# Optimization experiments

Measured on AMD Instinct MI355X. Metric: run time of the kernel, lower is better.

The kernel has to match this reference:

```python
import jax, jax.numpy as jnp
import numpy as np

B, S, D, H, DFF = 4, 2048, 1024, 16, 4096
HD = D // H
EPS = 1e-12

def _layernorm(x, g, b):
    mu = jnp.mean(x, axis=-1, keepdims=True)
    var = jnp.mean(jnp.square(x - mu), axis=-1, keepdims=True)
    return (x - mu) * jax.lax.rsqrt(var + EPS) * g + b

def setup_inputs() -> dict:
    key = jax.random.key(0)
    ks = jax.random.split(key, 12)
    sd = 0.02
    inp = {
        'hidden_states': jax.random.normal(ks[0], (B, S, D), jnp.float32),
        'attention_mask': jnp.zeros((B, 1, 1, S), jnp.float32),
        'Wq': jax.random.normal(ks[1], (D, D), jnp.float32) * sd,
        'bq': jnp.zeros((D,), jnp.float32),
        'Wk': jax.random.normal(ks[2], (D, D), jnp.float32) * sd,
        'bk': jnp.zeros((D,), jnp.float32),
        'Wv': jax.random.normal(ks[3], (D, D), jnp.float32) * sd,
        'bv': jnp.zeros((D,), jnp.float32),
        'Wo': jax.random.normal(ks[4], (D, D), jnp.float32) * sd,
        'bo': jnp.zeros((D,), jnp.float32),
        'ln1_g': jnp.ones((D,), jnp.float32),
        'ln1_b': jnp.zeros((D,), jnp.float32),
        'Wi': jax.random.normal(ks[5], (D, DFF), jnp.float32) * sd,
        'bi': jnp.zeros((DFF,), jnp.float32),
        'Wo2': jax.random.normal(ks[6], (DFF, D), jnp.float32) * sd,
        'bo2': jnp.zeros((D,), jnp.float32),
        'ln2_g': jnp.ones((D,), jnp.float32),
        'ln2_b': jnp.zeros((D,), jnp.float32),
    }
    return inp

def reference(hidden_states, attention_mask, Wq, bq, Wk, bk, Wv, bv, Wo, bo,
              ln1_g, ln1_b, Wi, bi, Wo2, bo2, ln2_g, ln2_b):
    x = hidden_states  # [B,S,D]
    # project and split heads -> [B,H,S,hd]
    def heads(t):
        return t.reshape(B, S, H, HD).transpose(0, 2, 1, 3)
    q = heads(x @ Wq + bq)
    k = heads(x @ Wk + bk)
    v = heads(x @ Wv + bv)
    scores = jnp.einsum('bhqd,bhkd->bhqk', q, k) / np.float32(np.sqrt(HD))
    scores = scores + attention_mask  # additive mask broadcast [B,1,1,S]
    weights = jax.nn.softmax(scores, axis=-1)
    ctx = jnp.einsum('bhqk,bhkd->bhqd', weights, v)
    ctx = ctx.transpose(0, 2, 1, 3).reshape(B, S, D)
    attn_out = _layernorm(ctx @ Wo + bo + x, ln1_g, ln1_b)
    # FFN (gelu) with residual + LayerNorm
    h = jax.nn.gelu(attn_out @ Wi + bi, approximate=False)
    out = _layernorm(h @ Wo2 + bo2 + attn_out, ln2_g, ln2_b)
    return out
```

## Files before the change

### kernel.cpp

```cpp
#include <hip/hip_runtime.h>
#include <hip/hip_bf16.h>
#include <math.h>

#define B_   4
#define S_   2048
#define D_   1024
#define H_   16
#define HD_  64
#define DFF_ 4096
#define M_   (B_*S_)

typedef __bf16 bf16x8 __attribute__((ext_vector_type(8)));
typedef __bf16 bf16x4 __attribute__((ext_vector_type(4)));
typedef float  floatx4 __attribute__((ext_vector_type(4)));

__device__ __forceinline__ float  b2f(__bf16 v) { return (float)v; }
__device__ __forceinline__ __bf16 f2b(float v)  { return (__bf16)v; }

__device__ __forceinline__ void async_ld16(const void* g, void* l) {
    __builtin_amdgcn_global_load_lds(
        (const __attribute__((address_space(1))) unsigned int*)g,
        (__attribute__((address_space(3))) unsigned int*)l, 16, 0, 0);
}

__global__ void transpose_conv_kernel(const float* __restrict__ in,
                                      __bf16* __restrict__ out, int R, int C,
                                      float scale)
{
    __shared__ float t[32][33];
    int c0 = blockIdx.x * 32, r0 = blockIdx.y * 32;
    int tx = threadIdx.x, ty = threadIdx.y;
    for (int i = ty; i < 32; i += 8)
        t[i][tx] = in[(long)(r0 + i) * C + c0 + tx];
    __syncthreads();
    for (int i = ty; i < 32; i += 8)
        out[(long)(c0 + i) * R + r0 + tx] = f2b(t[tx][i] * scale);
}

__global__ void vt_transpose_kernel(const __bf16* __restrict__ qkv,
                                    __bf16* __restrict__ vtg)
{
    __shared__ __bf16 t[32][34];
    int b  = blockIdx.z;
    int h  = blockIdx.y >> 1;
    int d0 = (blockIdx.y & 1) * 32;
    int s0 = blockIdx.x * 32;
    int tx = threadIdx.x, ty = threadIdx.y;
    for (int i = ty; i < 32; i += 8)
        t[i][tx] = qkv[(long)(b * S_ + s0 + i) * 3072 + 2048 + h * 64 + d0 + tx];
    __syncthreads();
    for (int i = ty; i < 32; i += 8)
        vtg[((long)(b * H_ + h) * 64 + d0 + i) * S_ + s0 + tx] = t[tx][i];
}

__global__ void f2b_kernel(const float* __restrict__ in, __bf16* __restrict__ out,
                           long n)
{
    long i = ((long)blockIdx.x * 256 + threadIdx.x) * 8;
    if (i >= n) return;
    float4 a = *(const float4*)&in[i];
    float4 c = *(const float4*)&in[i + 4];
    union { __bf16 h[8]; uint4 u; } p;
    p.h[0] = f2b(a.x); p.h[1] = f2b(a.y); p.h[2] = f2b(a.z); p.h[3] = f2b(a.w);
    p.h[4] = f2b(c.x); p.h[5] = f2b(c.y); p.h[6] = f2b(c.z); p.h[7] = f2b(c.w);
    *(uint4*)&out[i] = p.u;
}

__global__ void bias_concat_kernel(const float* __restrict__ bq,
                                   const float* __restrict__ bk,
                                   const float* __restrict__ bv,
                                   float* __restrict__ dst)
{
    int i = blockIdx.x * 256 + threadIdx.x;
    if (i >= 3 * D_) return;
    float v = (i < D_) ? bq[i] * 0.125f
            : (i < 2 * D_) ? bk[i - D_] : bv[i - 2 * D_];
    dst[i] = v;
}

template<int MODE>
__global__ __launch_bounds__(256, 2)
void gemm_kernel(const __bf16* __restrict__ A, const __bf16* __restrict__ Bt,
                 const float* __restrict__ bias, const float* __restrict__ resid,
                 float* __restrict__ Cf, __bf16* __restrict__ Cb,
                 int M, int N, int K)
{
    __shared__ __bf16 sA[128 * 64];
    __shared__ __bf16 sB[128 * 64];

    const int tid  = threadIdx.x;
    const int lane = tid & 63;
    const int wave = tid >> 6;
    const int wm   = (wave >> 1) * 64;
    const int wn   = (wave & 1) * 64;
    const long bm  = (long)blockIdx.y * 128;
    const long bn  = (long)blockIdx.x * 128;

    floatx4 acc[4][4];
#pragma unroll
    for (int i = 0; i < 4; ++i)
#pragma unroll
        for (int j = 0; j < 4; ++j)
#pragma unroll
            for (int r = 0; r < 4; ++r) acc[i][j][r] = 0.0f;

    const int mrow = lane & 15;
    const int quad = lane >> 4;
    const int koff0 = ((0 * 4 + quad) ^ (mrow & 7)) * 8;
    const int koff1 = ((1 * 4 + quad) ^ (mrow & 7)) * 8;

    for (int k0 = 0; k0 < K; k0 += 64) {
        __syncthreads();
#pragma unroll
        for (int t = 0; t < 4; ++t) {
            int ci  = tid + t * 256;
            int row = ci >> 3;
            int col = ((ci & 7) ^ (row & 7)) << 3;
            async_ld16(A  + (bm + row) * (long)K + k0 + col, &sA[ci * 8]);
            async_ld16(Bt + (bn + row) * (long)K + k0 + col, &sB[ci * 8]);
        }
        __syncthreads();

#pragma unroll
        for (int s = 0; s < 2; ++s) {
            const int ko = s ? koff1 : koff0;
            bf16x8 a[4], b[4];
#pragma unroll
            for (int i = 0; i < 4; ++i)
                a[i] = *(const bf16x8*)&sA[(wm + i * 16 + mrow) * 64 + ko];
#pragma unroll
            for (int j = 0; j < 4; ++j)
                b[j] = *(const bf16x8*)&sB[(wn + j * 16 + mrow) * 64 + ko];
#pragma unroll
            for (int i = 0; i < 4; ++i)
#pragma unroll
                for (int j = 0; j < 4; ++j)
                    acc[i][j] = __builtin_amdgcn_mfma_f32_16x16x32_bf16(
                        a[i], b[j], acc[i][j], 0, 0, 0);
        }
    }

    const int rq = quad * 4;
    const int cn = lane & 15;
#pragma unroll
    for (int i = 0; i < 4; ++i) {
#pragma unroll
        for (int j = 0; j < 4; ++j) {
            long col = bn + wn + j * 16 + cn;
            float bv = bias[col];
#pragma unroll
            for (int r = 0; r < 4; ++r) {
                long row = bm + wm + i * 16 + rq + r;
                float v = acc[i][j][r] + bv;
                if (MODE == 0) {
                    Cb[row * N + col] = f2b(v);
                } else if (MODE == 1) {
                    Cf[row * N + col] = v + resid[row * N + col];
                } else {
                    float g = 0.5f * v * (1.0f + erff(v * 0.70710678118654752f));
                    Cb[row * N + col] = f2b(g);
                }
            }
        }
    }
}

__global__ __launch_bounds__(256, 2)
void attn_kernel(const __bf16* __restrict__ QKV, const __bf16* __restrict__ VT,
                 const float* __restrict__ mask, __bf16* __restrict__ ctx)
{
    __shared__ __bf16 Qs[64 * 64];
    __shared__ __bf16 Ks[64 * 64];
    __shared__ __bf16 Vt[64 * 64];
    __shared__ __bf16 Ps[64 * 64];

    const int tid  = threadIdx.x;
    const int lane = tid & 63;
    const int wave = tid >> 6;
    const int w16  = wave * 16;
    const int b    = blockIdx.z, h = blockIdx.y;
    const int q0   = blockIdx.x * 64;
    const int cn   = lane & 15;
    const int quad = lane >> 4;
    const int rq   = quad * 4;
    const int koff0 = ((0 * 4 + quad) ^ (cn & 7)) * 8;
    const int koff1 = ((1 * 4 + quad) ^ (cn & 7)) * 8;

#pragma unroll
    for (int t = 0; t < 2; ++t) {
        int ci = tid + t * 256;
        int qr = ci >> 3, dc = ((ci & 7) ^ (qr & 7)) << 3;
        async_ld16(QKV + (long)(b * S_ + q0 + qr) * 3072 + h * 64 + dc,
                   &Qs[ci * 8]);
    }
    __syncthreads();
    const bf16x8 aq0 = *(const bf16x8*)&Qs[(w16 + cn) * 64 + koff0];
    const bf16x8 aq1 = *(const bf16x8*)&Qs[(w16 + cn) * 64 + koff1];

    float l_[4];
    floatx4 o_[4];
#pragma unroll
    for (int r = 0; r < 4; ++r) l_[r] = 0.0f;
#pragma unroll
    for (int jt = 0; jt < 4; ++jt)
#pragma unroll
        for (int r = 0; r < 4; ++r) o_[jt][r] = 0.0f;

    const long vbase = ((long)(b * H_ + h) * 64) * S_;

    for (int k0 = 0; k0 < S_; k0 += 64) {
        __syncthreads();
#pragma unroll
        for (int t = 0; t < 2; ++t) {
            int ci = tid + t * 256;
            int kr = ci >> 3, dc = ((ci & 7) ^ (kr & 7)) << 3;
            async_ld16(QKV + (long)(b * S_ + k0 + kr) * 3072 + 1024 + h * 64 + dc,
                       &Ks[ci * 8]);
            int vd = ci >> 3, kc = ((ci & 7) ^ (vd & 7)) << 3;
            async_ld16(VT + vbase + (long)vd * S_ + k0 + kc, &Vt[ci * 8]);
        }
        __syncthreads();

        floatx4 st[4];
#pragma unroll
        for (int jt = 0; jt < 4; ++jt)
#pragma unroll
            for (int r = 0; r < 4; ++r) st[jt][r] = 0.0f;
#pragma unroll
        for (int jt = 0; jt < 4; ++jt) {
            bf16x8 b0 = *(const bf16x8*)&Ks[(jt * 16 + cn) * 64 + koff0];
            bf16x8 b1 = *(const bf16x8*)&Ks[(jt * 16 + cn) * 64 + koff1];
            st[jt] = __builtin_amdgcn_mfma_f32_16x16x32_bf16(aq0, b0, st[jt], 0, 0, 0);
            st[jt] = __builtin_amdgcn_mfma_f32_16x16x32_bf16(aq1, b1, st[jt], 0, 0, 0);
        }
#pragma unroll
        for (int jt = 0; jt < 4; ++jt) {
            float mv = mask[(long)b * S_ + k0 + jt * 16 + cn] - 8.0f;
#pragma unroll
            for (int r = 0; r < 4; ++r) {
                float p = __expf(st[jt][r] + mv);
                st[jt][r] = p;
                l_[r] += p;
            }
        }
#pragma unroll
        for (int jt = 0; jt < 4; ++jt)
#pragma unroll
            for (int r = 0; r < 4; ++r) {
                int prow = w16 + rq + r;
                int pcol = (((jt * 2 + (cn >> 3)) ^ (prow & 7)) << 3) + (cn & 7);
                Ps[prow * 64 + pcol] = f2b(st[jt][r]);
            }

        {
            bf16x8 ap0 = *(const bf16x8*)&Ps[(w16 + cn) * 64 + koff0];
            bf16x8 ap1 = *(const bf16x8*)&Ps[(w16 + cn) * 64 + koff1];
#pragma unroll
            for (int jt = 0; jt < 4; ++jt) {
                bf16x8 b0 = *(const bf16x8*)&Vt[(jt * 16 + cn) * 64 + koff0];
                bf16x8 b1 = *(const bf16x8*)&Vt[(jt * 16 + cn) * 64 + koff1];
                o_[jt] = __builtin_amdgcn_mfma_f32_16x16x32_bf16(ap0, b0, o_[jt], 0, 0, 0);
                o_[jt] = __builtin_amdgcn_mfma_f32_16x16x32_bf16(ap1, b1, o_[jt], 0, 0, 0);
            }
        }
    }

#pragma unroll
    for (int r = 0; r < 4; ++r) {
        float l = l_[r];
        l += __shfl_xor(l, 1);
        l += __shfl_xor(l, 2);
        l += __shfl_xor(l, 4);
        l += __shfl_xor(l, 8);
        float linv = 1.0f / l;
        long rowg = (long)(b * S_ + q0 + w16 + rq + r) * D_ + h * 64;
#pragma unroll
        for (int jt = 0; jt < 4; ++jt)
            ctx[rowg + jt * 16 + cn] = f2b(o_[jt][r] * linv);
    }
}

__global__ __launch_bounds__(256)
void ln_kernel(const float* __restrict__ X, const float* __restrict__ gamma,
               const float* __restrict__ beta, float* __restrict__ out,
               __bf16* __restrict__ outb)
{
    const long row = blockIdx.x;
    const int tid = threadIdx.x;
    const float* x = X + row * D_;
    float4 v = *(const float4*)&x[tid * 4];
    float s  = v.x + v.y + v.z + v.w;
    float s2 = v.x * v.x + v.y * v.y + v.z * v.z + v.w * v.w;
    for (int off = 32; off > 0; off >>= 1) {
        s  += __shfl_down(s, off);
        s2 += __shfl_down(s2, off);
    }
    __shared__ float red[8];
    int wave = tid >> 6, lane = tid & 63;
    if (lane == 0) { red[wave] = s; red[4 + wave] = s2; }
    __syncthreads();
    float ts  = red[0] + red[1] + red[2] + red[3];
    float ts2 = red[4] + red[5] + red[6] + red[7];
    float mu  = ts * (1.0f / D_);
    float var = ts2 * (1.0f / D_) - mu * mu;
    float rs  = rsqrtf(fmaxf(var, 0.0f) + 1e-12f);
    float4 g = *(const float4*)&gamma[tid * 4];
    float4 b = *(const float4*)&beta[tid * 4];
    float4 o;
    o.x = (v.x - mu) * rs * g.x + b.x;
    o.y = (v.y - mu) * rs * g.y + b.y;
    o.z = (v.z - mu) * rs * g.z + b.z;
    o.w = (v.w - mu) * rs * g.w + b.w;
    *(float4*)&out[row * D_ + tid * 4] = o;
    if (outb) {
        bf16x4 ob;
        ob[0] = f2b(o.x); ob[1] = f2b(o.y); ob[2] = f2b(o.z); ob[3] = f2b(o.w);
        *(bf16x4*)&outb[row * D_ + tid * 4] = ob;
    }
}

extern "C" void kernel_launch(void* const* d_in, const int* in_sizes, int n_in,
                              void* d_out, int out_size, void* d_ws, size_t ws_size,
                              hipStream_t stream)
{
    const float* hid  = (const float*)d_in[0];
    const float* mask = (const float*)d_in[1];
    const float* Wq   = (const float*)d_in[2];
    const float* bq   = (const float*)d_in[3];
    const float* Wk   = (const float*)d_in[4];
    const float* bk   = (const float*)d_in[5];
    const float* Wv   = (const float*)d_in[6];
    const float* bv   = (const float*)d_in[7];
    const float* Wo   = (const float*)d_in[8];
    const float* bo   = (const float*)d_in[9];
    const float* g1   = (const float*)d_in[10];
    const float* b1   = (const float*)d_in[11];
    const float* Wi   = (const float*)d_in[12];
    const float* bi   = (const float*)d_in[13];
    const float* Wo2  = (const float*)d_in[14];
    const float* bo2  = (const float*)d_in[15];
    const float* g2   = (const float*)d_in[16];
    const float* b2   = (const float*)d_in[17];
    float* out = (float*)d_out;

    char* w = (char*)d_ws;
    auto take = [&](size_t bytes) { char* p = w; w += bytes; return p; };
    __bf16* wqkvb = (__bf16*)take((size_t)3 * D_ * D_ * 2);
    __bf16* wob   = (__bf16*)take((size_t)D_ * D_ * 2);
    __bf16* wib   = (__bf16*)take((size_t)D_ * DFF_ * 2);
    __bf16* wo2b  = (__bf16*)take((size_t)D_ * DFF_ * 2);
    float*  qkvbias = (float*)take(16384);
    __bf16* qkv   = (__bf16*)take((size_t)M_ * 3 * D_ * 2);
    __bf16* ctxb  = (__bf16*)take((size_t)M_ * D_ * 2);
    __bf16* hb    = (__bf16*)take((size_t)M_ * D_ * 2);
    float*  tmp      = (float*)take((size_t)M_ * D_ * 4);
    float*  attn_out = (float*)take((size_t)M_ * D_ * 4);
    __bf16* hbuf = qkv;
    __bf16* vtg  = hb;
    __bf16* attn_out_b = hb;
    (void)in_sizes; (void)n_in; (void)out_size; (void)ws_size;

    dim3 tb(32, 8);
    transpose_conv_kernel<<<dim3(D_/32, D_/32), tb, 0, stream>>>(Wq, wqkvb,            D_, D_, 0.125f);
    transpose_conv_kernel<<<dim3(D_/32, D_/32), tb, 0, stream>>>(Wk, wqkvb + D_*D_,    D_, D_, 1.0f);
    transpose_conv_kernel<<<dim3(D_/32, D_/32), tb, 0, stream>>>(Wv, wqkvb + 2*D_*D_,  D_, D_, 1.0f);
    transpose_conv_kernel<<<dim3(D_/32, D_/32), tb, 0, stream>>>(Wo, wob, D_, D_, 1.0f);
    transpose_conv_kernel<<<dim3(DFF_/32, D_/32), tb, 0, stream>>>(Wi, wib, D_, DFF_, 1.0f);
    transpose_conv_kernel<<<dim3(D_/32, DFF_/32), tb, 0, stream>>>(Wo2, wo2b, DFF_, D_, 1.0f);
    bias_concat_kernel<<<12, 256, 0, stream>>>(bq, bk, bv, qkvbias);
    f2b_kernel<<<(M_*D_/8 + 255)/256, 256, 0, stream>>>(hid, hb, (long)M_*D_);

    gemm_kernel<0><<<dim3(3*D_/128, M_/128), 256, 0, stream>>>(
        hb, wqkvb, qkvbias, nullptr, nullptr, qkv, M_, 3*D_, D_);

    vt_transpose_kernel<<<dim3(S_/32, H_*2, B_), tb, 0, stream>>>(qkv, vtg);

    attn_kernel<<<dim3(S_/64, H_, B_), 256, 0, stream>>>(qkv, vtg, mask, ctxb);

    gemm_kernel<1><<<dim3(D_/128, M_/128), 256, 0, stream>>>(
        ctxb, wob, bo, hid, tmp, nullptr, M_, D_, D_);
    ln_kernel<<<M_, 256, 0, stream>>>(tmp, g1, b1, attn_out, attn_out_b);

    gemm_kernel<2><<<dim3(DFF_/128, M_/128), 256, 0, stream>>>(
        attn_out_b, wib, bi, nullptr, nullptr, hbuf, M_, DFF_, D_);
    gemm_kernel<1><<<dim3(D_/128, M_/128), 256, 0, stream>>>(
        hbuf, wo2b, bo2, attn_out, tmp, nullptr, M_, D_, DFF_);
    ln_kernel<<<M_, 256, 0, stream>>>(tmp, g2, b2, out, nullptr);
}
```

Before: 611.4 us.

## Double-buffer K/V tiles and process 128 queries per attention block

The attention kernel now handles 128 query rows per block (32 per wave, two 16-row MFMA tiles), so each K/V tile loaded into shared memory is reused across twice as many queries. K/V staging is double-buffered: the next tile's async loads are issued before computing on the current one, with one barrier per iteration instead of two. Q is read straight from global memory into registers instead of going through shared memory. In exchange, register pressure and shared memory per block go up, and the grid is half as large (512 blocks), which may reduce occupancy.

```diff
diff --git a/kernel.cpp b/kernel.cpp
--- a/kernel.cpp
+++ b/kernel.cpp
@@ -169,115 +169,152 @@
 void attn_kernel(const __bf16* __restrict__ QKV, const __bf16* __restrict__ VT,
                  const float* __restrict__ mask, __bf16* __restrict__ ctx)
 {
-    __shared__ __bf16 Qs[64 * 64];
-    __shared__ __bf16 Ks[64 * 64];
-    __shared__ __bf16 Vt[64 * 64];
-    __shared__ __bf16 Ps[64 * 64];
+    __shared__ __bf16 Ks[2][64 * 64];
+    __shared__ __bf16 Vt[2][64 * 64];
+    __shared__ __bf16 Ps[128 * 64];
 
     const int tid  = threadIdx.x;
     const int lane = tid & 63;
     const int wave = tid >> 6;
-    const int w16  = wave * 16;
+    const int wq   = wave * 32;
     const int b    = blockIdx.z, h = blockIdx.y;
-    const int q0   = blockIdx.x * 64;
+    const int q0   = blockIdx.x * 128;
     const int cn   = lane & 15;
     const int quad = lane >> 4;
     const int rq   = quad * 4;
     const int koff0 = ((0 * 4 + quad) ^ (cn & 7)) * 8;
     const int koff1 = ((1 * 4 + quad) ^ (cn & 7)) * 8;
 
-#pragma unroll
-    for (int t = 0; t < 2; ++t) {
-        int ci = tid + t * 256;
-        int qr = ci >> 3, dc = ((ci & 7) ^ (qr & 7)) << 3;
-        async_ld16(QKV + (long)(b * S_ + q0 + qr) * 3072 + h * 64 + dc,
-                   &Qs[ci * 8]);
-    }
-    __syncthreads();
-    const bf16x8 aq0 = *(const bf16x8*)&Qs[(w16 + cn) * 64 + koff0];
-    const bf16x8 aq1 = *(const bf16x8*)&Qs[(w16 + cn) * 64 + koff1];
-
-    float l_[4];
-    floatx4 o_[4];
-#pragma unroll
-    for (int r = 0; r < 4; ++r) l_[r] = 0.0f;
-#pragma unroll
-    for (int jt = 0; jt < 4; ++jt)
-#pragma unroll
-        for (int r = 0; r < 4; ++r) o_[jt][r] = 0.0f;
+    bf16x8 aq0[2], aq1[2];
+#pragma unroll
+    for (int it = 0; it < 2; ++it) {
+        const __bf16* qp =
+            QKV + (long)(b * S_ + q0 + wq + it * 16 + cn) * 3072 + h * 64;
+        aq0[it] = *(const bf16x8*)(qp + quad * 8);
+        aq1[it] = *(const bf16x8*)(qp + 32 + quad * 8);
+    }
+
+    float l_[2][4];
+    floatx4 o_[2][4];
+#pragma unroll
+    for (int it = 0; it < 2; ++it) {
+#pragma unroll
+        for (int r = 0; r < 4; ++r) l_[it][r] = 0.0f;
+#pragma unroll
+        for (int jt = 0; jt < 4; ++jt)
+#pragma unroll
+            for (int r = 0; r < 4; ++r) o_[it][jt][r] = 0.0f;
+    }
 
     const long vbase = ((long)(b * H_ + h) * 64) * S_;
 
-    for (int k0 = 0; k0 < S_; k0 += 64) {
-        __syncthreads();
+    auto STAGE = [&](int bufi, int k0) {
 #pragma unroll
         for (int t = 0; t < 2; ++t) {
             int ci = tid + t * 256;
-            int kr = ci >> 3, dc = ((ci & 7) ^ (kr & 7)) << 3;
-            async_ld16(QKV + (long)(b * S_ + k0 + kr) * 3072 + 1024 + h * 64 + dc,
-                       &Ks[ci * 8]);
-            int vd = ci >> 3, kc = ((ci & 7) ^ (vd & 7)) << 3;
-            async_ld16(VT + vbase + (long)vd * S_ + k0 + kc, &Vt[ci * 8]);
-        }
-        __syncthreads();
-
-        floatx4 st[4];
-#pragma unroll
-        for (int jt = 0; jt < 4; ++jt)
-#pragma unroll
-            for (int r = 0; r < 4; ++r) st[jt][r] = 0.0f;
+            int r  = ci >> 3;
+            int cz = ((ci & 7) ^ (r & 7)) << 3;
+            async_ld16(QKV + (long)(b * S_ + k0 + r) * 3072 + 1024 + h * 64 + cz,
+                       &Ks[bufi][ci * 8]);
+            async_ld16(VT + vbase + (long)r * S_ + k0 + cz, &Vt[bufi][ci * 8]);
+        }
+    };
+
+    STAGE(0, 0);
+    asm volatile("s_waitcnt vmcnt(0)" ::: "memory");
+    __builtin_amdgcn_s_barrier();
+    __builtin_amdgcn_sched_barrier(0);
+
+    int cur = 0;
+    for (int k0 = 0; k0 < S_; k0 += 64) {
+        if (k0 + 64 < S_) STAGE(cur ^ 1, k0 + 64);
+
+        floatx4 st[2][4];
+#pragma unroll
+        for (int it = 0; it < 2; ++it)
+#pragma unroll
+            for (int jt = 0; jt < 4; ++jt)
+#pragma unroll
+                for (int r = 0; r < 4; ++r) st[it][jt][r] = 0.0f;
 #pragma unroll
         for (int jt = 0; jt < 4; ++jt) {
-            bf16x8 b0 = *(const bf16x8*)&Ks[(jt * 16 + cn) * 64 + koff0];
-            bf16x8 b1 = *(const bf16x8*)&Ks[(jt * 16 + cn) * 64 + koff1];
-            st[jt] = __builtin_amdgcn_mfma_f32_16x16x32_bf16(aq0, b0, st[jt], 0, 0, 0);
-            st[jt] = __builtin_amdgcn_mfma_f32_16x16x32_bf16(aq1, b1, st[jt], 0, 0, 0);
-        }
+            bf16x8 kb0 = *(const bf16x8*)&Ks[cur][(jt * 16 + cn) * 64 + koff0];
+            bf16x8 kb1 = *(const bf16x8*)&Ks[cur][(jt * 16 + cn) * 64 + koff1];
+#pragma unroll
+            for (int it = 0; it < 2; ++it) {
+                st[it][jt] = __builtin_amdgcn_mfma_f32_16x16x32_bf16(
+                    aq0[it], kb0, st[it][jt], 0, 0, 0);
+                st[it][jt] = __builtin_amdgcn_mfma_f32_16x16x32_bf16(
+                    aq1[it], kb1, st[it][jt], 0, 0, 0);
+            }
+        }
+
 #pragma unroll
         for (int jt = 0; jt < 4; ++jt) {
             float mv = mask[(long)b * S_ + k0 + jt * 16 + cn] - 8.0f;
 #pragma unroll
-            for (int r = 0; r < 4; ++r) {
-                float p = __expf(st[jt][r] + mv);
-                st[jt][r] = p;
-                l_[r] += p;
+            for (int it = 0; it < 2; ++it)
+#pragma unroll
+                for (int r = 0; r < 4; ++r) {
+                    float p = __expf(st[it][jt][r] + mv);
+                    st[it][jt][r] = p;
+                    l_[it][r] += p;
+                }
+        }
+
+#pragma unroll
+        for (int it = 0; it < 2; ++it)
+#pragma unroll
+            for (int jt = 0; jt < 4; ++jt)
+#pragma unroll
+                for (int r = 0; r < 4; ++r) {
+                    int prow = wq + it * 16 + rq + r;
+                    int pcol = (((jt * 2 + (cn >> 3)) ^ (prow & 7)) << 3) + (cn & 7);
+                    Ps[prow * 64 + pcol] = f2b(st[it][jt][r]);
+                }
+
+        {
+            bf16x8 ap0[2], ap1[2];
+#pragma unroll
+            for (int it = 0; it < 2; ++it) {
+                ap0[it] = *(const bf16x8*)&Ps[(wq + it * 16 + cn) * 64 + koff0];
+                ap1[it] = *(const bf16x8*)&Ps[(wq + it * 16 + cn) * 64 + koff1];
             }
-        }
-#pragma unroll
-        for (int jt = 0; jt < 4; ++jt)
-#pragma unroll
-            for (int r = 0; r < 4; ++r) {
-                int prow = w16 + rq + r;
-                int pcol = (((jt * 2 + (cn >> 3)) ^ (prow & 7)) << 3) + (cn & 7);
-                Ps[prow * 64 + pcol] = f2b(st[jt][r]);
+#pragma unroll
+            for (int jt = 0; jt < 4; ++jt) {
+                bf16x8 vb0 = *(const bf16x8*)&Vt[cur][(jt * 16 + cn) * 64 + koff0];
+                bf16x8 vb1 = *(const bf16x8*)&Vt[cur][(jt * 16 + cn) * 64 + koff1];
+#pragma unroll
+                for (int it = 0; it < 2; ++it) {
+                    o_[it][jt] = __builtin_amdgcn_mfma_f32_16x16x32_bf16(
+                        ap0[it], vb0, o_[it][jt], 0, 0, 0);
+                    o_[it][jt] = __builtin_amdgcn_mfma_f32_16x16x32_bf16(
+                        ap1[it], vb1, o_[it][jt], 0, 0, 0);
+                }
             }
-
-        {
-            bf16x8 ap0 = *(const bf16x8*)&Ps[(w16 + cn) * 64 + koff0];
-            bf16x8 ap1 = *(const bf16x8*)&Ps[(w16 + cn) * 64 + koff1];
-#pragma unroll
-            for (int jt = 0; jt < 4; ++jt) {
-                bf16x8 b0 = *(const bf16x8*)&Vt[(jt * 16 + cn) * 64 + koff0];
-                bf16x8 b1 = *(const bf16x8*)&Vt[(jt * 16 + cn) * 64 + koff1];
-                o_[jt] = __builtin_amdgcn_mfma_f32_16x16x32_bf16(ap0, b0, o_[jt], 0, 0, 0);
-                o_[jt] = __builtin_amdgcn_mfma_f32_16x16x32_bf16(ap1, b1, o_[jt], 0, 0, 0);
-            }
-        }
-    }
-
-#pragma unroll
-    for (int r = 0; r < 4; ++r) {
-        float l = l_[r];
-        l += __shfl_xor(l, 1);
-        l += __shfl_xor(l, 2);
-        l += __shfl_xor(l, 4);
-        l += __shfl_xor(l, 8);
-        float linv = 1.0f / l;
-        long rowg = (long)(b * S_ + q0 + w16 + rq + r) * D_ + h * 64;
-#pragma unroll
-        for (int jt = 0; jt < 4; ++jt)
-            ctx[rowg + jt * 16 + cn] = f2b(o_[jt][r] * linv);
-    }
+        }
+
+        asm volatile("s_waitcnt vmcnt(0) lgkmcnt(0)" ::: "memory");
+        __builtin_amdgcn_s_barrier();
+        __builtin_amdgcn_sched_barrier(0);
+        cur ^= 1;
+    }
+
+#pragma unroll
+    for (int it = 0; it < 2; ++it)
+#pragma unroll
+        for (int r = 0; r < 4; ++r) {
+            float l = l_[it][r];
+            l += __shfl_xor(l, 1);
+            l += __shfl_xor(l, 2);
+            l += __shfl_xor(l, 4);
+            l += __shfl_xor(l, 8);
+            float linv = 1.0f / l;
+            long rowg = (long)(b * S_ + q0 + wq + it * 16 + rq + r) * D_ + h * 64;
+#pragma unroll
+            for (int jt = 0; jt < 4; ++jt)
+                ctx[rowg + jt * 16 + cn] = f2b(o_[it][jt][r] * linv);
+        }
 }
 
 __global__ __launch_bounds__(256)
@@ -375,7 +412,7 @@
 
     vt_transpose_kernel<<<dim3(S_/32, H_*2, B_), tb, 0, stream>>>(qkv, vtg);
 
-    attn_kernel<<<dim3(S_/64, H_, B_), 256, 0, stream>>>(qkv, vtg, mask, ctxb);
+    attn_kernel<<<dim3(S_/128, H_, B_), 256, 0, stream>>>(qkv, vtg, mask, ctxb);
 
     gemm_kernel<1><<<dim3(D_/128, M_/128), 256, 0, stream>>>(
         ctxb, wob, bo, hid, tmp, nullptr, M_, D_, D_);
```

Measured after the change: 618.1 us. No clear change (+1.1%).

## Add 256x256-tile 8-wave GEMM with ping-pong LDS staging for QKV and FFN-up

Applied to the files above, without the earlier changes.

Adds a new GEMM kernel using 256x256 output tiles, 512 threads (8 waves), double-buffered LDS filled by async global-to-LDS loads with an XOR swizzle, and an XCD-aware remapping of block IDs. Each iteration splits the tile into four quadrant MFMA phases, interleaving the next tile's loads with compute, and raises wave priority during MFMA bursts. It is used for the QKV projection and the FFN up-projection with GELU. Larger tiles raise arithmetic intensity and cut global traffic, at the cost of fewer blocks (grid of 12x32 and 16x32) and heavy LDS use (128KB), which can cost occupancy and wave balance.

```diff
diff --git a/kernel.cpp b/kernel.cpp
--- a/kernel.cpp
+++ b/kernel.cpp
@@ -160,6 +160,177 @@
                     float g = 0.5f * v * (1.0f + erff(v * 0.70710678118654752f));
                     Cb[row * N + col] = f2b(g);
                 }
+            }
+        }
+    }
+}
+
+template<int MODE>
+__global__ __launch_bounds__(512, 2)
+void gemm256_kernel(const __bf16* __restrict__ A, const __bf16* __restrict__ Bt,
+                    const float* __restrict__ bias, const float* __restrict__ resid,
+                    float* __restrict__ Cf, __bf16* __restrict__ Cb,
+                    int M, int N, int K)
+{
+    __shared__ __bf16 sA[2][256 * 64];
+    __shared__ __bf16 sB[2][256 * 64];
+
+    const int nbx = gridDim.x;
+    const int nwg = nbx * gridDim.y;
+    const int orig = blockIdx.y * nbx + blockIdx.x;
+    const int q8 = nwg >> 3, r8 = nwg & 7, xcd = orig & 7, off = orig >> 3;
+    const int wg = (xcd < r8 ? xcd * (q8 + 1) : r8 * (q8 + 1) + (xcd - r8) * q8) + off;
+    const long bm = (long)(wg / nbx) * 256;
+    const long bn = (long)(wg % nbx) * 256;
+
+    const int tid  = threadIdx.x;
+    const int lane = tid & 63;
+    const int wave = tid >> 6;
+    const int g    = wave >> 2;
+    const int c    = wave & 3;
+    const int cn   = lane & 15;
+    const int quad = lane >> 4;
+    const int rq   = quad * 4;
+
+    floatx4 acc[2][2][4][2];
+#pragma unroll
+    for (int qi = 0; qi < 2; ++qi)
+#pragma unroll
+    for (int qj = 0; qj < 2; ++qj)
+#pragma unroll
+    for (int i = 0; i < 4; ++i)
+#pragma unroll
+    for (int j = 0; j < 2; ++j)
+#pragma unroll
+        for (int r = 0; r < 4; ++r) acc[qi][qj][i][j][r] = 0.0f;
+
+    const int NT = K >> 6;
+
+    auto STAGE = [&](int pb, int isB, int half, int t) {
+        const __bf16* src = isB ? Bt : A;
+        const long    base = isB ? bn : bm;
+        __bf16*       dst  = isB ? &sB[pb][0] : &sA[pb][0];
+        const int k0 = t << 6;
+#pragma unroll
+        for (int tt = 0; tt < 2; ++tt) {
+            int ci  = tid + tt * 512;
+            int row = (ci >> 3) + half * 128;
+            int col = ((ci & 7) ^ (row & 7)) << 3;
+            async_ld16(src + (base + row) * (long)K + k0 + col,
+                       dst + half * 8192 + ci * 8);
+        }
+    };
+    auto LDA = [&](int pb, int qi, bf16x8 (&a)[2][4]) {
+#pragma unroll
+        for (int i = 0; i < 4; ++i) {
+            int rr = g * 64 + qi * 128 + i * 16 + cn;
+#pragma unroll
+            for (int s = 0; s < 2; ++s) {
+                int ko = ((s * 4 + quad) ^ (rr & 7)) << 3;
+                a[s][i] = *(const bf16x8*)&sA[pb][rr * 64 + ko];
+            }
+        }
+    };
+    auto LDB = [&](int pb, int qj, bf16x8 (&b)[2][2]) {
+#pragma unroll
+        for (int j = 0; j < 2; ++j) {
+            int rr = c * 32 + qj * 128 + j * 16 + cn;
+#pragma unroll
+            for (int s = 0; s < 2; ++s) {
+                int ko = ((s * 4 + quad) ^ (rr & 7)) << 3;
+                b[s][j] = *(const bf16x8*)&sB[pb][rr * 64 + ko];
+            }
+        }
+    };
+    auto MM = [&](bf16x8 (&a)[2][4], bf16x8 (&b)[2][2], floatx4 (&ac)[4][2]) {
+#pragma unroll
+        for (int s = 0; s < 2; ++s)
+#pragma unroll
+        for (int i = 0; i < 4; ++i)
+#pragma unroll
+        for (int j = 0; j < 2; ++j)
+            ac[i][j] = __builtin_amdgcn_mfma_f32_16x16x32_bf16(
+                a[s][i], b[s][j], ac[i][j], 0, 0, 0);
+    };
+
+    STAGE(0, 0, 0, 0); STAGE(0, 1, 0, 0); STAGE(0, 1, 1, 0); STAGE(0, 0, 1, 0);
+    STAGE(1, 0, 0, 1); STAGE(1, 1, 1, 1);
+    asm volatile("s_waitcnt vmcnt(4)" ::: "memory");
+    __builtin_amdgcn_s_barrier();
+    __builtin_amdgcn_sched_barrier(0);
+
+    bf16x8 a[2][4], b[2][2];
+    for (int t = 0; t < NT; ++t) {
+        const int pb = t & 1;
+        LDA(pb, 0, a); LDB(pb, 0, b);
+        if (t + 1 < NT) STAGE(pb ^ 1, 0, 1, t + 1);
+        asm volatile("s_waitcnt lgkmcnt(8)" ::: "memory");
+        __builtin_amdgcn_s_barrier();
+        asm volatile("s_waitcnt lgkmcnt(0)" ::: "memory");
+        __builtin_amdgcn_sched_barrier(0);
+        __builtin_amdgcn_s_setprio(1);
+        MM(a, b, acc[0][0]);
+        __builtin_amdgcn_s_setprio(0);
+        __builtin_amdgcn_s_barrier();
+        __builtin_amdgcn_sched_barrier(0);
+        LDB(pb, 1, b);
+        if (t + 1 < NT) STAGE(pb ^ 1, 1, 0, t + 1);
+        __builtin_amdgcn_s_barrier();
+        asm volatile("s_waitcnt lgkmcnt(0)" ::: "memory");
+        __builtin_amdgcn_sched_barrier(0);
+        __builtin_amdgcn_s_setprio(1);
+        MM(a, b, acc[0][1]);
+        __builtin_amdgcn_s_setprio(0);
+        __builtin_amdgcn_s_barrier();
+        __builtin_amdgcn_sched_barrier(0);
+        LDA(pb, 1, a);
+        if (t + 2 < NT) STAGE(pb, 0, 0, t + 2);
+        __builtin_amdgcn_s_barrier();
+        asm volatile("s_waitcnt lgkmcnt(0)" ::: "memory");
+        __builtin_amdgcn_sched_barrier(0);
+        __builtin_amdgcn_s_setprio(1);
+        MM(a, b, acc[1][1]);
+        __builtin_amdgcn_s_setprio(0);
+        __builtin_amdgcn_s_barrier();
+        __builtin_amdgcn_sched_barrier(0);
+        LDB(pb, 0, b);
+        if (t + 2 < NT) STAGE(pb, 1, 1, t + 2);
+        if (t + 1 < NT) {
+            asm volatile("s_waitcnt vmcnt(4)" ::: "memory");
+        } else {
+            asm volatile("s_waitcnt vmcnt(0)" ::: "memory");
+        }
+        __builtin_amdgcn_s_barrier();
+        asm volatile("s_waitcnt lgkmcnt(0)" ::: "memory");
+        __builtin_amdgcn_sched_barrier(0);
+        __builtin_amdgcn_s_setprio(1);
+        MM(a, b, acc[1][0]);
+        __builtin_amdgcn_s_setprio(0);
+        __builtin_amdgcn_s_barrier();
+        __builtin_amdgcn_sched_barrier(0);
+    }
+
+#pragma unroll
+    for (int qi = 0; qi < 2; ++qi)
+#pragma unroll
+    for (int i = 0; i < 4; ++i)
+#pragma unroll
+    for (int qj = 0; qj < 2; ++qj)
+#pragma unroll
+    for (int j = 0; j < 2; ++j) {
+        long col = bn + c * 32 + qj * 128 + j * 16 + cn;
+        float bv = bias[col];
+#pragma unroll
+        for (int r = 0; r < 4; ++r) {
+            long row = bm + g * 64 + qi * 128 + i * 16 + rq + r;
+            float v = acc[qi][qj][i][j][r] + bv;
+            if (MODE == 0) {
+                Cb[row * N + col] = f2b(v);
+            } else if (MODE == 1) {
+                Cf[row * N + col] = v + resid[row * N + col];
+            } else {
+                float ge = 0.5f * v * (1.0f + erff(v * 0.70710678118654752f));
+                Cb[row * N + col] = f2b(ge);
             }
         }
     }
@@ -370,7 +541,7 @@
     bias_concat_kernel<<<12, 256, 0, stream>>>(bq, bk, bv, qkvbias);
     f2b_kernel<<<(M_*D_/8 + 255)/256, 256, 0, stream>>>(hid, hb, (long)M_*D_);
 
-    gemm_kernel<0><<<dim3(3*D_/128, M_/128), 256, 0, stream>>>(
+    gemm256_kernel<0><<<dim3(3*D_/256, M_/256), 512, 0, stream>>>(
         hb, wqkvb, qkvbias, nullptr, nullptr, qkv, M_, 3*D_, D_);
 
     vt_transpose_kernel<<<dim3(S_/32, H_*2, B_), tb, 0, stream>>>(qkv, vtg);
@@ -381,7 +552,7 @@
         ctxb, wob, bo, hid, tmp, nullptr, M_, D_, D_);
     ln_kernel<<<M_, 256, 0, stream>>>(tmp, g1, b1, attn_out, attn_out_b);
 
-    gemm_kernel<2><<<dim3(DFF_/128, M_/128), 256, 0, stream>>>(
+    gemm256_kernel<2><<<dim3(DFF_/256, M_/256), 512, 0, stream>>>(
         attn_out_b, wib, bi, nullptr, nullptr, hbuf, M_, DFF_, D_);
     gemm_kernel<1><<<dim3(D_/128, M_/128), 256, 0, stream>>>(
         hbuf, wo2b, bo2, attn_out, tmp, nullptr, M_, D_, DFF_);
```

After: 622.8 us. Within noise of the previous version (+1.9%).

## Double-buffer K/V tiles in attention kernel to overlap loads with MFMA

Applied to the files above, without the earlier changes.

The attention kernel now keeps two shared-memory buffers for K and V and prefetches the next tile asynchronously while the current one is being computed. Each iteration ends with a single explicit waitcnt and barrier instead of two __syncthreads calls. The Q tile is staged through the P buffer, so total LDS use stays at 40KB instead of growing. The goal is to hide global-load latency behind the QK and PV MFMAs, at the cost of relying on hand-placed waitcnt and barriers for correctness.

```diff
diff --git a/kernel.cpp b/kernel.cpp
--- a/kernel.cpp
+++ b/kernel.cpp
@@ -169,9 +169,8 @@
 void attn_kernel(const __bf16* __restrict__ QKV, const __bf16* __restrict__ VT,
                  const float* __restrict__ mask, __bf16* __restrict__ ctx)
 {
-    __shared__ __bf16 Qs[64 * 64];
-    __shared__ __bf16 Ks[64 * 64];
-    __shared__ __bf16 Vt[64 * 64];
+    __shared__ __bf16 Ks[2][64 * 64];
+    __shared__ __bf16 Vt[2][64 * 64];
     __shared__ __bf16 Ps[64 * 64];
 
     const int tid  = threadIdx.x;
@@ -186,16 +185,34 @@
     const int koff0 = ((0 * 4 + quad) ^ (cn & 7)) * 8;
     const int koff1 = ((1 * 4 + quad) ^ (cn & 7)) * 8;
 
+    const long vbase = ((long)(b * H_ + h) * 64) * S_;
+
+    auto STAGE = [&](int bufi, int k0) {
+#pragma unroll
+        for (int t = 0; t < 2; ++t) {
+            int ci = tid + t * 256;
+            int r  = ci >> 3;
+            int cz = ((ci & 7) ^ (r & 7)) << 3;
+            async_ld16(QKV + (long)(b * S_ + k0 + r) * 3072 + 1024 + h * 64 + cz,
+                       &Ks[bufi][ci * 8]);
+            async_ld16(VT + vbase + (long)r * S_ + k0 + cz, &Vt[bufi][ci * 8]);
+        }
+    };
+
 #pragma unroll
     for (int t = 0; t < 2; ++t) {
         int ci = tid + t * 256;
         int qr = ci >> 3, dc = ((ci & 7) ^ (qr & 7)) << 3;
         async_ld16(QKV + (long)(b * S_ + q0 + qr) * 3072 + h * 64 + dc,
-                   &Qs[ci * 8]);
-    }
-    __syncthreads();
-    const bf16x8 aq0 = *(const bf16x8*)&Qs[(w16 + cn) * 64 + koff0];
-    const bf16x8 aq1 = *(const bf16x8*)&Qs[(w16 + cn) * 64 + koff1];
+                   &Ps[ci * 8]);
+    }
+    STAGE(0, 0);
+    asm volatile("s_waitcnt vmcnt(0)" ::: "memory");
+    __builtin_amdgcn_s_barrier();
+    __builtin_amdgcn_sched_barrier(0);
+
+    const bf16x8 aq0 = *(const bf16x8*)&Ps[(w16 + cn) * 64 + koff0];
+    const bf16x8 aq1 = *(const bf16x8*)&Ps[(w16 + cn) * 64 + koff1];
 
     float l_[4];
     floatx4 o_[4];
@@ -206,20 +223,9 @@
 #pragma unroll
         for (int r = 0; r < 4; ++r) o_[jt][r] = 0.0f;
 
-    const long vbase = ((long)(b * H_ + h) * 64) * S_;
-
+    int cur = 0;
     for (int k0 = 0; k0 < S_; k0 += 64) {
-        __syncthreads();
-#pragma unroll
-        for (int t = 0; t < 2; ++t) {
-            int ci = tid + t * 256;
-            int kr = ci >> 3, dc = ((ci & 7) ^ (kr & 7)) << 3;
-            async_ld16(QKV + (long)(b * S_ + k0 + kr) * 3072 + 1024 + h * 64 + dc,
-                       &Ks[ci * 8]);
-            int vd = ci >> 3, kc = ((ci & 7) ^ (vd & 7)) << 3;
-            async_ld16(VT + vbase + (long)vd * S_ + k0 + kc, &Vt[ci * 8]);
-        }
-        __syncthreads();
+        if (k0 + 64 < S_) STAGE(cur ^ 1, k0 + 64);
 
         floatx4 st[4];
 #pragma unroll
@@ -228,8 +234,8 @@
             for (int r = 0; r < 4; ++r) st[jt][r] = 0.0f;
 #pragma unroll
         for (int jt = 0; jt < 4; ++jt) {
-            bf16x8 b0 = *(const bf16x8*)&Ks[(jt * 16 + cn) * 64 + koff0];
-            bf16x8 b1 = *(const bf16x8*)&Ks[(jt * 16 + cn) * 64 + koff1];
+            bf16x8 b0 = *(const bf16x8*)&Ks[cur][(jt * 16 + cn) * 64 + koff0];
+            bf16x8 b1 = *(const bf16x8*)&Ks[cur][(jt * 16 + cn) * 64 + koff1];
             st[jt] = __builtin_amdgcn_mfma_f32_16x16x32_bf16(aq0, b0, st[jt], 0, 0, 0);
             st[jt] = __builtin_amdgcn_mfma_f32_16x16x32_bf16(aq1, b1, st[jt], 0, 0, 0);
         }
@@ -257,12 +263,17 @@
             bf16x8 ap1 = *(const bf16x8*)&Ps[(w16 + cn) * 64 + koff1];
 #pragma unroll
             for (int jt = 0; jt < 4; ++jt) {
-                bf16x8 b0 = *(const bf16x8*)&Vt[(jt * 16 + cn) * 64 + koff0];
-                bf16x8 b1 = *(const bf16x8*)&Vt[(jt * 16 + cn) * 64 + koff1];
+                bf16x8 b0 = *(const bf16x8*)&Vt[cur][(jt * 16 + cn) * 64 + koff0];
+                bf16x8 b1 = *(const bf16x8*)&Vt[cur][(jt * 16 + cn) * 64 + koff1];
                 o_[jt] = __builtin_amdgcn_mfma_f32_16x16x32_bf16(ap0, b0, o_[jt], 0, 0, 0);
                 o_[jt] = __builtin_amdgcn_mfma_f32_16x16x32_bf16(ap1, b1, o_[jt], 0, 0, 0);
             }
         }
+
+        asm volatile("s_waitcnt vmcnt(0) lgkmcnt(0)" ::: "memory");
+        __builtin_amdgcn_s_barrier();
+        __builtin_amdgcn_sched_barrier(0);
+        cur ^= 1;
     }
 
 #pragma unroll
```

New measurement: 569.0 us. 1.07x faster.
